# Performance work log

Measured on AMD Instinct MI355X. Metric: run time of the kernel, lower is better.

Reference implementation:

```python
import jax, jax.numpy as jnp
import numpy as np

NODE_SIZE = 500000
LINK_SIZE = 500
DIM = 128
NORM_P = 1
MARGIN = 1.0
BATCH = 16384


def setup_inputs() -> dict:
    key = jax.random.key(0)
    k1, k2, k3, k4, k5, k6, k7, k8 = jax.random.split(key, 8)
    ur_e = 6.0 / np.sqrt(DIM)
    ur_m = 6.0 / DIM
    node_w = jax.random.uniform(k1, (NODE_SIZE, DIM), jnp.float32, -ur_e, ur_e)
    link_w = jax.random.uniform(k2, (LINK_SIZE, DIM), jnp.float32, -ur_e, ur_e)
    transfer_w = jax.random.uniform(k3, (LINK_SIZE, DIM * DIM), jnp.float32, -ur_m, ur_m)
    sp = jax.random.randint(k4, (BATCH,), 0, NODE_SIZE)
    tp = jax.random.randint(k5, (BATCH,), 0, NODE_SIZE)
    sn = jax.random.randint(k6, (BATCH,), 0, NODE_SIZE)
    tn = jax.random.randint(k7, (BATCH,), 0, NODE_SIZE)
    r = jax.random.randint(k8, (BATCH,), 0, LINK_SIZE)
    return {"node_w": node_w, "link_w": link_w, "transfer_w": transfer_w,
            "sp": sp, "tp": tp, "sn": sn, "tn": tn, "r": r}


def _distance(node_w, link_w, transfer_w, s, r, t):
    # gather embeddings
    s_emb = node_w[s]                      # [B, D]
    t_emb = node_w[t]                      # [B, D]
    r_emb = link_w[r]                      # [B, D]
    M = transfer_w[r].reshape(-1, DIM, DIM)  # [B, D, D]
    # per-sample (1xD)x(DxD) matvec: e @ M
    s_proj = jnp.einsum('bd,bde->be', s_emb, M)
    t_proj = jnp.einsum('bd,bde->be', t_emb, M)
    diff = s_proj + r_emb - t_proj
    if NORM_P == 1:
        return jnp.sum(jnp.abs(diff), axis=1)
    return jnp.sum(jnp.abs(diff) ** NORM_P, axis=1) ** (1.0 / NORM_P)


def reference(node_w, link_w, transfer_w, sp, tp, sn, tn, r):
    pos = _distance(node_w, link_w, transfer_w, sp, r, tp)
    neg = _distance(node_w, link_w, transfer_w, sn, r, tn)
    # MarginRankingLoss with target = -1: max(0, (pos - neg) + margin)
    loss = jnp.maximum(pos - neg + MARGIN, 0.0)
    return jnp.mean(loss)
```

## Files before the change

### kernel.cpp

```cpp
#include <hip/hip_runtime.h>

#define BATCH 16384
#define DIM 128
#define NLINK 500
#define EHALF 64
#define NS 16
#define DP_STRIDE 132
#define CAP 128

#define WS_COUNTS 0
#define WS_BUCKET 512
#define WS_P0 (512 + NLINK * CAP)
#define WS_P1 (WS_P0 + BATCH)
#define WS_N0 (WS_P1 + BATCH)
#define WS_N1 (WS_N0 + BATCH)

__global__ void k_zero(int* wsi, float* out) {
    int t = threadIdx.x;
    wsi[WS_COUNTS + t] = 0;
    if (t == 0) out[0] = 0.0f;
}

__global__ void k_scatter(const int* __restrict__ r, int* wsi) {
    int i = blockIdx.x * blockDim.x + threadIdx.x;
    if (i < BATCH) {
        int rr = r[i];
        int pos = atomicAdd(&wsi[WS_COUNTS + rr], 1);
        wsi[WS_BUCKET + rr * CAP + pos] = i;
    }
}

__global__ __launch_bounds__(256, 3) void k_main(
    const float* __restrict__ node_w, const float* __restrict__ link_w,
    const float* __restrict__ transfer_w,
    const int* __restrict__ sp, const int* __restrict__ tp,
    const int* __restrict__ sn, const int* __restrict__ tn,
    int* __restrict__ wsi)
{
    __shared__ float Ms[DIM * EHALF];
    __shared__ float dp[NS * DP_STRIDE];
    __shared__ float dn[NS * DP_STRIDE];
    __shared__ float remb[EHALF];

    const int link = blockIdx.x >> 1;
    const int h = blockIdx.x & 1;
    const int t = threadIdx.x;

    {
        const float4* G = (const float4*)transfer_w;
        float4* Ms4 = (float4*)Ms;
        #pragma unroll
        for (int i = 0; i < 8; i++) {
            int c = t + 256 * i;
            Ms4[c] = G[link * 4096 + (c >> 4) * 32 + h * 16 + (c & 15)];
        }
    }
    if (t < 16)
        ((float4*)remb)[t] = ((const float4*)(link_w + link * DIM + h * EHALF))[t];

    const int count = wsi[WS_COUNTS + link];
    const int base  = WS_BUCKET + link * CAP;
    const int g = t >> 4;
    const int q = t & 15;
    float* dpr = dp + g * DP_STRIDE;
    float* dnr = dn + g * DP_STRIDE;
    float* pOut = (float*)(wsi + (h ? WS_P1 : WS_P0));
    float* nOut = (float*)(wsi + (h ? WS_N1 : WS_N0));

    __syncthreads();

    for (int k = 0; k < count; k += NS) {
        const int myk = k + g;
        const bool active = (myk < count);
        int b = 0;
        if (active) {
            b = wsi[base + myk];
            const float4* a  = (const float4*)(node_w + (size_t)sp[b] * DIM);
            const float4* c2 = (const float4*)(node_w + (size_t)tp[b] * DIM);
            float4 a0 = a[q], a1 = a[q + 16], c0 = c2[q], c1 = c2[q + 16];
            float4 w0, w1;
            w0.x = a0.x - c0.x; w0.y = a0.y - c0.y; w0.z = a0.z - c0.z; w0.w = a0.w - c0.w;
            w1.x = a1.x - c1.x; w1.y = a1.y - c1.y; w1.z = a1.z - c1.z; w1.w = a1.w - c1.w;
            ((float4*)dpr)[q] = w0;
            ((float4*)dpr)[q + 16] = w1;
            const float4* e2 = (const float4*)(node_w + (size_t)sn[b] * DIM);
            const float4* f2 = (const float4*)(node_w + (size_t)tn[b] * DIM);
            float4 e0 = e2[q], e1 = e2[q + 16], f0 = f2[q], f1 = f2[q + 16];
            w0.x = e0.x - f0.x; w0.y = e0.y - f0.y; w0.z = e0.z - f0.z; w0.w = e0.w - f0.w;
            w1.x = e1.x - f1.x; w1.y = e1.y - f1.y; w1.z = e1.z - f1.z; w1.w = e1.w - f1.w;
            ((float4*)dnr)[q] = w0;
            ((float4*)dnr)[q + 16] = w1;
        }
        __syncthreads();

        float4 accp = {0.f, 0.f, 0.f, 0.f};
        float4 accn = {0.f, 0.f, 0.f, 0.f};
        const float4* M4 = (const float4*)Ms;
        #pragma unroll 4
        for (int d4 = 0; d4 < 32; d4++) {
            float4 vp = ((const float4*)dpr)[d4];
            float4 vn = ((const float4*)dnr)[d4];
            float4 m0 = M4[(4 * d4 + 0) * 16 + q];
            float4 m1 = M4[(4 * d4 + 1) * 16 + q];
            float4 m2 = M4[(4 * d4 + 2) * 16 + q];
            float4 m3 = M4[(4 * d4 + 3) * 16 + q];
            accp.x = fmaf(m0.x, vp.x, accp.x); accp.y = fmaf(m0.y, vp.x, accp.y);
            accp.z = fmaf(m0.z, vp.x, accp.z); accp.w = fmaf(m0.w, vp.x, accp.w);
            accn.x = fmaf(m0.x, vn.x, accn.x); accn.y = fmaf(m0.y, vn.x, accn.y);
            accn.z = fmaf(m0.z, vn.x, accn.z); accn.w = fmaf(m0.w, vn.x, accn.w);
            accp.x = fmaf(m1.x, vp.y, accp.x); accp.y = fmaf(m1.y, vp.y, accp.y);
            accp.z = fmaf(m1.z, vp.y, accp.z); accp.w = fmaf(m1.w, vp.y, accp.w);
            accn.x = fmaf(m1.x, vn.y, accn.x); accn.y = fmaf(m1.y, vn.y, accn.y);
            accn.z = fmaf(m1.z, vn.y, accn.z); accn.w = fmaf(m1.w, vn.y, accn.w);
            accp.x = fmaf(m2.x, vp.z, accp.x); accp.y = fmaf(m2.y, vp.z, accp.y);
            accp.z = fmaf(m2.z, vp.z, accp.z); accp.w = fmaf(m2.w, vp.z, accp.w);
            accn.x = fmaf(m2.x, vn.z, accn.x); accn.y = fmaf(m2.y, vn.z, accn.y);
            accn.z = fmaf(m2.z, vn.z, accn.z); accn.w = fmaf(m2.w, vn.z, accn.w);
            accp.x = fmaf(m3.x, vp.w, accp.x); accp.y = fmaf(m3.y, vp.w, accp.y);
            accp.z = fmaf(m3.z, vp.w, accp.z); accp.w = fmaf(m3.w, vp.w, accp.w);
            accn.x = fmaf(m3.x, vn.w, accn.x); accn.y = fmaf(m3.y, vn.w, accn.y);
            accn.z = fmaf(m3.z, vn.w, accn.z); accn.w = fmaf(m3.w, vn.w, accn.w);
        }

        float4 re = ((const float4*)remb)[q];
        float lp = fabsf(accp.x + re.x) + fabsf(accp.y + re.y) +
                   fabsf(accp.z + re.z) + fabsf(accp.w + re.w);
        float ln = fabsf(accn.x + re.x) + fabsf(accn.y + re.y) +
                   fabsf(accn.z + re.z) + fabsf(accn.w + re.w);
        #pragma unroll
        for (int o = 8; o >= 1; o >>= 1) {
            lp += __shfl_xor(lp, o, 16);
            ln += __shfl_xor(ln, o, 16);
        }
        if (active && q == 0) {
            pOut[b] = lp;
            nOut[b] = ln;
        }
        __syncthreads();
    }
}

__global__ void k_final(const int* __restrict__ wsi, float* __restrict__ out) {
    const float* p0 = (const float*)(wsi + WS_P0);
    const float* p1 = (const float*)(wsi + WS_P1);
    const float* n0 = (const float*)(wsi + WS_N0);
    const float* n1 = (const float*)(wsi + WS_N1);
    int i = blockIdx.x * 256 + threadIdx.x;
    float l = 0.0f;
    if (i < BATCH) {
        float pos = p0[i] + p1[i];
        float neg = n0[i] + n1[i];
        l = fmaxf(pos - neg + 1.0f, 0.0f);
    }
    #pragma unroll
    for (int o = 32; o >= 1; o >>= 1) l += __shfl_xor(l, o, 64);
    __shared__ float w[4];
    if ((threadIdx.x & 63) == 0) w[threadIdx.x >> 6] = l;
    __syncthreads();
    if (threadIdx.x == 0)
        atomicAdd(out, (w[0] + w[1] + w[2] + w[3]) * (1.0f / BATCH));
}

extern "C" void kernel_launch(void* const* d_in, const int* in_sizes, int n_in,
                              void* d_out, int out_size, void* d_ws, size_t ws_size,
                              hipStream_t stream) {
    const float* node_w     = (const float*)d_in[0];
    const float* link_w     = (const float*)d_in[1];
    const float* transfer_w = (const float*)d_in[2];
    const int* sp = (const int*)d_in[3];
    const int* tp = (const int*)d_in[4];
    const int* sn = (const int*)d_in[5];
    const int* tn = (const int*)d_in[6];
    const int* r  = (const int*)d_in[7];
    float* out = (float*)d_out;
    int* wsi = (int*)d_ws;

    k_zero<<<1, 512, 0, stream>>>(wsi, out);
    k_scatter<<<(BATCH + 255) / 256, 256, 0, stream>>>(r, wsi);
    k_main<<<NLINK * 2, 256, 0, stream>>>(node_w, link_w, transfer_w,
                                          sp, tp, sn, tn, wsi);
    k_final<<<(BATCH + 255) / 256, 256, 0, stream>>>(wsi, out);
}
```

Before: 350.3 us.

## Build per-wave link buckets in-kernel and drop scatter kernels and block barriers

Removes the zero and atomic scatter kernels. Each block now scans the whole relation index array with wave ballots and builds per-wave local buckets of the samples that use its link. Each wave then processes its own samples independently, so the per-iteration block barriers go away. The transfer matrix slice is loaded straight into LDS with global_load_lds, and the final reduction becomes a single 1024-thread block that writes the result without atomics. In exchange, every block rereads the full index array, and the per-wave bucket capacity of 64 is assumed to be enough.

New measurement: 354.9 us. About the same (+1.3%).

```diff
diff --git a/kernel.cpp b/kernel.cpp
--- a/kernel.cpp
+++ b/kernel.cpp
@@ -4,77 +4,91 @@
 #define DIM 128
 #define NLINK 500
 #define EHALF 64
-#define NS 16
 #define DP_STRIDE 132
-#define CAP 128
-
-#define WS_COUNTS 0
-#define WS_BUCKET 512
-#define WS_P0 (512 + NLINK * CAP)
-#define WS_P1 (WS_P0 + BATCH)
-#define WS_N0 (WS_P1 + BATCH)
-#define WS_N1 (WS_N0 + BATCH)
-
-__global__ void k_zero(int* wsi, float* out) {
-    int t = threadIdx.x;
-    wsi[WS_COUNTS + t] = 0;
-    if (t == 0) out[0] = 0.0f;
-}
-
-__global__ void k_scatter(const int* __restrict__ r, int* wsi) {
-    int i = blockIdx.x * blockDim.x + threadIdx.x;
-    if (i < BATCH) {
-        int rr = r[i];
-        int pos = atomicAdd(&wsi[WS_COUNTS + rr], 1);
-        wsi[WS_BUCKET + rr * CAP + pos] = i;
-    }
-}
+#define CAPW 64
+
+#define WS_P0 0
+#define WS_P1 BATCH
+#define WS_N0 (2 * BATCH)
+#define WS_N1 (3 * BATCH)
+
+typedef __attribute__((address_space(1))) const unsigned int ga_u32;
+typedef __attribute__((address_space(3))) unsigned int ls_u32;
 
 __global__ __launch_bounds__(256, 3) void k_main(
     const float* __restrict__ node_w, const float* __restrict__ link_w,
     const float* __restrict__ transfer_w,
     const int* __restrict__ sp, const int* __restrict__ tp,
     const int* __restrict__ sn, const int* __restrict__ tn,
-    int* __restrict__ wsi)
+    const int* __restrict__ r, float* __restrict__ wsf)
 {
     __shared__ float Ms[DIM * EHALF];
-    __shared__ float dp[NS * DP_STRIDE];
-    __shared__ float dn[NS * DP_STRIDE];
+    __shared__ float dp[16 * DP_STRIDE];
+    __shared__ float dn[16 * DP_STRIDE];
     __shared__ float remb[EHALF];
+    __shared__ int lbucket[4 * CAPW];
 
     const int link = blockIdx.x >> 1;
     const int h = blockIdx.x & 1;
     const int t = threadIdx.x;
+    const int w = t >> 6;
+    const int lane = t & 63;
 
     {
-        const float4* G = (const float4*)transfer_w;
-        float4* Ms4 = (float4*)Ms;
+        const float4* gbase = (const float4*)transfer_w + (size_t)link * 4096 + h * 16;
         #pragma unroll
         for (int i = 0; i < 8; i++) {
             int c = t + 256 * i;
-            Ms4[c] = G[link * 4096 + (c >> 4) * 32 + h * 16 + (c & 15)];
+            const float4* gp = gbase + (c >> 4) * 32 + (c & 15);
+            __builtin_amdgcn_global_load_lds((ga_u32*)gp, (ls_u32*)(Ms + 4 * c), 16, 0, 0);
         }
     }
     if (t < 16)
         ((float4*)remb)[t] = ((const float4*)(link_w + link * DIM + h * EHALF))[t];
 
-    const int count = wsi[WS_COUNTS + link];
-    const int base  = WS_BUCKET + link * CAP;
-    const int g = t >> 4;
-    const int q = t & 15;
-    float* dpr = dp + g * DP_STRIDE;
-    float* dnr = dn + g * DP_STRIDE;
-    float* pOut = (float*)(wsi + (h ? WS_P1 : WS_P0));
-    float* nOut = (float*)(wsi + (h ? WS_N1 : WS_N0));
+    int cw = 0;
+    {
+        const int4* r4 = (const int4*)r;
+        int* myb = lbucket + w * CAPW;
+        const unsigned long long ltmask = (lane == 63) ? ~0ull >> 1
+                                                       : (1ull << lane) - 1;
+        #pragma unroll 4
+        for (int it = 0; it < 16; it++) {
+            int gi = w * 1024 + it * 64 + lane;
+            int4 v = r4[gi];
+            int base4 = gi * 4;
+            unsigned long long m;
+            m = __ballot(v.x == link);
+            if (v.x == link) myb[cw + __popcll(m & ltmask)] = base4 + 0;
+            cw += __popcll(m);
+            m = __ballot(v.y == link);
+            if (v.y == link) myb[cw + __popcll(m & ltmask)] = base4 + 1;
+            cw += __popcll(m);
+            m = __ballot(v.z == link);
+            if (v.z == link) myb[cw + __popcll(m & ltmask)] = base4 + 2;
+            cw += __popcll(m);
+            m = __ballot(v.w == link);
+            if (v.w == link) myb[cw + __popcll(m & ltmask)] = base4 + 3;
+            cw += __popcll(m);
+        }
+    }
 
     __syncthreads();
 
-    for (int k = 0; k < count; k += NS) {
-        const int myk = k + g;
-        const bool active = (myk < count);
+    const int g16 = lane >> 4;
+    const int q = lane & 15;
+    float* dpr = dp + (w * 4 + g16) * DP_STRIDE;
+    float* dnr = dn + (w * 4 + g16) * DP_STRIDE;
+    float* pOut = wsf + (h ? WS_P1 : WS_P0);
+    float* nOut = wsf + (h ? WS_N1 : WS_N0);
+    const int* myb = lbucket + w * CAPW;
+
+    for (int k = 0; k < cw; k += 4) {
+        const int myk = k + g16;
+        const bool active = (myk < cw);
         int b = 0;
         if (active) {
-            b = wsi[base + myk];
+            b = myb[myk];
             const float4* a  = (const float4*)(node_w + (size_t)sp[b] * DIM);
             const float4* c2 = (const float4*)(node_w + (size_t)tp[b] * DIM);
             float4 a0 = a[q], a1 = a[q + 16], c0 = c2[q], c1 = c2[q + 16];
@@ -91,7 +105,6 @@
             ((float4*)dnr)[q] = w0;
             ((float4*)dnr)[q + 16] = w1;
         }
-        __syncthreads();
 
         float4 accp = {0.f, 0.f, 0.f, 0.f};
         float4 accn = {0.f, 0.f, 0.f, 0.f};
@@ -136,29 +149,36 @@
             pOut[b] = lp;
             nOut[b] = ln;
         }
-        __syncthreads();
     }
 }
 
-__global__ void k_final(const int* __restrict__ wsi, float* __restrict__ out) {
-    const float* p0 = (const float*)(wsi + WS_P0);
-    const float* p1 = (const float*)(wsi + WS_P1);
-    const float* n0 = (const float*)(wsi + WS_N0);
-    const float* n1 = (const float*)(wsi + WS_N1);
-    int i = blockIdx.x * 256 + threadIdx.x;
-    float l = 0.0f;
-    if (i < BATCH) {
+__global__ __launch_bounds__(1024) void k_final(
+    const float* __restrict__ wsf, float* __restrict__ out)
+{
+    __shared__ float wred[16];
+    const int t = threadIdx.x;
+    const float* p0 = wsf + WS_P0;
+    const float* p1 = wsf + WS_P1;
+    const float* n0 = wsf + WS_N0;
+    const float* n1 = wsf + WS_N1;
+    float s = 0.0f;
+    #pragma unroll
+    for (int m = 0; m < BATCH / 1024; m++) {
+        int i = t + 1024 * m;
         float pos = p0[i] + p1[i];
         float neg = n0[i] + n1[i];
-        l = fmaxf(pos - neg + 1.0f, 0.0f);
+        s += fmaxf(pos - neg + 1.0f, 0.0f);
     }
     #pragma unroll
-    for (int o = 32; o >= 1; o >>= 1) l += __shfl_xor(l, o, 64);
-    __shared__ float w[4];
-    if ((threadIdx.x & 63) == 0) w[threadIdx.x >> 6] = l;
+    for (int o = 32; o >= 1; o >>= 1) s += __shfl_xor(s, o, 64);
+    if ((t & 63) == 0) wred[t >> 6] = s;
     __syncthreads();
-    if (threadIdx.x == 0)
-        atomicAdd(out, (w[0] + w[1] + w[2] + w[3]) * (1.0f / BATCH));
+    if (t == 0) {
+        float tot = 0.0f;
+        #pragma unroll
+        for (int i = 0; i < 16; i++) tot += wred[i];
+        out[0] = tot * (1.0f / BATCH);
+    }
 }
 
 extern "C" void kernel_launch(void* const* d_in, const int* in_sizes, int n_in,
@@ -173,11 +193,9 @@
     const int* tn = (const int*)d_in[6];
     const int* r  = (const int*)d_in[7];
     float* out = (float*)d_out;
-    int* wsi = (int*)d_ws;
-
-    k_zero<<<1, 512, 0, stream>>>(wsi, out);
-    k_scatter<<<(BATCH + 255) / 256, 256, 0, stream>>>(r, wsi);
+    float* wsf = (float*)d_ws;
+
     k_main<<<NLINK * 2, 256, 0, stream>>>(node_w, link_w, transfer_w,
-                                          sp, tp, sn, tn, wsi);
-    k_final<<<(BATCH + 255) / 256, 256, 0, stream>>>(wsi, out);
+                                          sp, tp, sn, tn, r, wsf);
+    k_final<<<1, 1024, 0, stream>>>(wsf, out);
 }
```
